# Kernel tuning notes

Hardware: AMD Instinct MI355X
Metric: run time of the kernel (lower is better)

## Reference

```python
import jax, jax.numpy as jnp
import numpy as np

K = 3  # kernel_size

def setup_inputs() -> dict:
    key = jax.random.key(0)
    k0, k1, k2 = jax.random.split(key, 3)
    B, C, H, W = 8, 128, 128, 128
    x = jax.random.normal(k0, (B, C, H, W), dtype=jnp.float32)
    # kernel_gen params: two 1x1 convs acting on a 1x1 pooled map -> plain matmuls
    w1 = jax.random.normal(k1, (C, C), dtype=jnp.float32) * 0.05          # conv1 weight [out,in]
    b1 = jnp.zeros((C,), dtype=jnp.float32)
    w2 = jax.random.normal(k2, (C * K * K, C), dtype=jnp.float32) * 0.05  # conv2 weight [out,in]
    b2 = jnp.zeros((C * K * K,), dtype=jnp.float32)
    return {"x": x, "w1": w1, "b1": b1, "w2": w2, "b2": b2}

def reference(x, w1, b1, w2, b2):
    B, C, H, W = x.shape
    k = K
    pad = k // 2
    # AdaptiveAvgPool2d(1) -> global mean; 1x1 convs -> matmuls on [B, C]
    pooled = x.mean(axis=(2, 3))                        # [B, C]
    h = jax.nn.relu(pooled @ w1.T + b1)                 # [B, C]
    kern = (h @ w2.T + b2).reshape(B, C, k * k)         # [B, C, k*k], channel-major = reshape(B*C,1,k,k)
    # Dynamic per-sample depthwise conv (cross-correlation, zero pad), via patches
    patches = jax.lax.conv_general_dilated_patches(
        x, (k, k), (1, 1), ((pad, pad), (pad, pad)),
        dimension_numbers=("NCHW", "OIHW", "NCHW"))     # [B, C*k*k, H, W], channel-major over (C, k, k)
    patches = patches.reshape(B, C, k * k, H, W)
    out = jnp.einsum("bcphw,bcp->bchw", patches, kern)  # [B, C, H, W]
    return out
```

## Files before the change

kernel.cpp:

```cpp
#include <hip/hip_runtime.h>

#define BB 8
#define CC 128
#define HH 128
#define WW 128
#define PLANE (HH * WW)
#define KK 9

__global__ __launch_bounds__(512) void pool_kernel(const float* __restrict__ x,
                                                   float* __restrict__ pooled) {
    int bc = blockIdx.x;
    const float4* p4 = (const float4*)(x + (size_t)bc * PLANE);
    int t = threadIdx.x;
    float s = 0.f;
#pragma unroll
    for (int i = 0; i < 8; ++i) {
        float4 v = p4[t + i * 512];
        s += v.x + v.y + v.z + v.w;
    }
#pragma unroll
    for (int off = 32; off > 0; off >>= 1) s += __shfl_down(s, off, 64);
    __shared__ float wsum[8];
    int wave = t >> 6, lane = t & 63;
    if (lane == 0) wsum[wave] = s;
    __syncthreads();
    if (t == 0) {
        float tot = 0.f;
#pragma unroll
        for (int i = 0; i < 8; ++i) tot += wsum[i];
        pooled[bc] = tot * (1.0f / PLANE);
    }
}

__global__ __launch_bounds__(128) void kerngen_kernel(const float* __restrict__ pooled,
                                                      const float* __restrict__ w1,
                                                      const float* __restrict__ b1,
                                                      const float* __restrict__ w2,
                                                      const float* __restrict__ b2,
                                                      float* __restrict__ kern) {
    int b = blockIdx.x / 9;
    int g = blockIdx.x % 9;
    int j = threadIdx.x;
    __shared__ float ps[CC];
    __shared__ float hs[CC];
    ps[j] = pooled[b * CC + j];
    __syncthreads();
    float acc = b1[j];
    const float* w1r = w1 + j * CC;
#pragma unroll 8
    for (int i = 0; i < CC; ++i) acc += ps[i] * w1r[i];
    hs[j] = fmaxf(acc, 0.f);
    __syncthreads();
    int o = g * CC + j;
    float acc2 = b2[o];
    const float* w2r = w2 + o * CC;
#pragma unroll 8
    for (int i = 0; i < CC; ++i) acc2 += hs[i] * w2r[i];
    kern[b * (CC * KK) + o] = acc2;
}

__global__ __launch_bounds__(256) void conv_kernel(const float* __restrict__ x,
                                                   const float* __restrict__ kern,
                                                   float* __restrict__ out) {
    int bid = blockIdx.x;
    int bc = bid >> 2, slice = bid & 3;
    const float* plane = x + (size_t)bc * PLANE;
    float* oplane = out + (size_t)bc * PLANE;
    const float* wp = kern + (size_t)bc * KK;
    float w[9];
#pragma unroll
    for (int p = 0; p < 9; ++p) w[p] = wp[p];

    int t = threadIdx.x;
    int xq = t & 31;
    int x0 = xq << 2;
    int yb = slice * 32 + (t >> 5) * 4;

    float4 A  = {0.f, 0.f, 0.f, 0.f};
    float4 Bv = {0.f, 0.f, 0.f, 0.f};

#pragma unroll
    for (int s = 0; s < 6; ++s) {
        int yr = yb - 1 + s;
        float4 cv = {0.f, 0.f, 0.f, 0.f};
        float l = 0.f, r = 0.f;
        if (yr >= 0 && yr < HH) {
            const float* row = plane + yr * WW;
            cv = *(const float4*)(row + x0);
            l = (xq > 0) ? row[x0 - 1] : 0.f;
            r = (xq < 31) ? row[x0 + 4] : 0.f;
        }
        float4 pbot, pmid, ptop;
        pbot.x = w[6]*l    + w[7]*cv.x + w[8]*cv.y;
        pbot.y = w[6]*cv.x + w[7]*cv.y + w[8]*cv.z;
        pbot.z = w[6]*cv.y + w[7]*cv.z + w[8]*cv.w;
        pbot.w = w[6]*cv.z + w[7]*cv.w + w[8]*r;
        pmid.x = w[3]*l    + w[4]*cv.x + w[5]*cv.y;
        pmid.y = w[3]*cv.x + w[4]*cv.y + w[5]*cv.z;
        pmid.z = w[3]*cv.y + w[4]*cv.z + w[5]*cv.w;
        pmid.w = w[3]*cv.z + w[4]*cv.w + w[5]*r;
        ptop.x = w[0]*l    + w[1]*cv.x + w[2]*cv.y;
        ptop.y = w[0]*cv.x + w[1]*cv.y + w[2]*cv.z;
        ptop.z = w[0]*cv.y + w[1]*cv.z + w[2]*cv.w;
        ptop.w = w[0]*cv.z + w[1]*cv.w + w[2]*r;

        A.x += pbot.x; A.y += pbot.y; A.z += pbot.z; A.w += pbot.w;
        int yo = yr - 1;
        if (yo >= yb && yo < yb + 4) {
            *(float4*)(oplane + yo * WW + x0) = A;
        }
        Bv.x += pmid.x; Bv.y += pmid.y; Bv.z += pmid.z; Bv.w += pmid.w;
        A = Bv;
        Bv = ptop;
    }
}

extern "C" void kernel_launch(void* const* d_in, const int* in_sizes, int n_in,
                              void* d_out, int out_size, void* d_ws, size_t ws_size,
                              hipStream_t stream) {
    const float* x  = (const float*)d_in[0];
    const float* w1 = (const float*)d_in[1];
    const float* b1 = (const float*)d_in[2];
    const float* w2 = (const float*)d_in[3];
    const float* b2 = (const float*)d_in[4];
    float* out = (float*)d_out;

    float* ws = (float*)d_ws;
    float* pooled = ws;
    float* kern   = ws + 1024;

    pool_kernel<<<BB * CC, 512, 0, stream>>>(x, pooled);
    kerngen_kernel<<<BB * 9, 128, 0, stream>>>(pooled, w1, b1, w2, b2, kern);
    conv_kernel<<<BB * CC * 4, 256, 0, stream>>>(x, kern, out);
}
```

Before: 138.0 us.

## Fuse pooling with kernel generation via last-block atomic counter; enlarge conv row tiles

Pooling and the kernel-generation MLP now run in one kernel. Each block publishes its plane sum, and the last block per batch, found with an atomic counter, computes the two matmuls for that batch. This removes one launch and the serial 72-block kerngen stage, at the cost of a memset launch and a single block doing each batch's 1152-output matmul. The conv kernel now has each thread produce 8 output rows instead of 4, halving the grid and cutting redundant halo-row loads.

Result: slower. 197.1 us (+42.8%).

```diff
diff --git a/kernel.cpp b/kernel.cpp
--- a/kernel.cpp
+++ b/kernel.cpp
@@ -7,64 +7,88 @@
 #define PLANE (HH * WW)
 #define KK 9
 
-__global__ __launch_bounds__(512) void pool_kernel(const float* __restrict__ x,
-                                                   float* __restrict__ pooled) {
+__global__ __launch_bounds__(512) void pool_kg_kernel(
+        const float* __restrict__ x,
+        const float* __restrict__ w1,
+        const float* __restrict__ b1,
+        const float* __restrict__ w2,
+        const float* __restrict__ b2,
+        float* __restrict__ psum,
+        int* __restrict__ counter,
+        float* __restrict__ kern) {
     int bc = blockIdx.x;
-    const float4* p4 = (const float4*)(x + (size_t)bc * PLANE);
+    int b = bc >> 7;
     int t = threadIdx.x;
+    __shared__ float wsum[8];
+    __shared__ int lastFlag;
+    __shared__ float ps[CC];
+    __shared__ float hs[CC];
+
+    const float4* g4 = (const float4*)(x + (size_t)bc * PLANE);
     float s = 0.f;
 #pragma unroll
     for (int i = 0; i < 8; ++i) {
-        float4 v = p4[t + i * 512];
+        float4 v = g4[t + i * 512];
         s += v.x + v.y + v.z + v.w;
     }
 #pragma unroll
     for (int off = 32; off > 0; off >>= 1) s += __shfl_down(s, off, 64);
-    __shared__ float wsum[8];
     int wave = t >> 6, lane = t & 63;
     if (lane == 0) wsum[wave] = s;
+    if (t == 0) lastFlag = 0;
     __syncthreads();
     if (t == 0) {
         float tot = 0.f;
 #pragma unroll
         for (int i = 0; i < 8; ++i) tot += wsum[i];
-        pooled[bc] = tot * (1.0f / PLANE);
+        __hip_atomic_store(&psum[bc], tot, __ATOMIC_RELEASE, __HIP_MEMORY_SCOPE_AGENT);
+        int old = __hip_atomic_fetch_add(&counter[b], 1, __ATOMIC_ACQ_REL,
+                                         __HIP_MEMORY_SCOPE_AGENT);
+        if (old == CC - 1) lastFlag = 1;
     }
-}
+    __syncthreads();
+    if (!lastFlag) return;
 
-__global__ __launch_bounds__(128) void kerngen_kernel(const float* __restrict__ pooled,
-                                                      const float* __restrict__ w1,
-                                                      const float* __restrict__ b1,
-                                                      const float* __restrict__ w2,
-                                                      const float* __restrict__ b2,
-                                                      float* __restrict__ kern) {
-    int b = blockIdx.x / 9;
-    int g = blockIdx.x % 9;
-    int j = threadIdx.x;
-    __shared__ float ps[CC];
-    __shared__ float hs[CC];
-    ps[j] = pooled[b * CC + j];
+    if (t < CC) {
+        float v = __hip_atomic_load(&psum[b * CC + t], __ATOMIC_ACQUIRE,
+                                    __HIP_MEMORY_SCOPE_AGENT);
+        ps[t] = v * (1.0f / PLANE);
+    }
     __syncthreads();
-    float acc = b1[j];
-    const float* w1r = w1 + j * CC;
-#pragma unroll 8
-    for (int i = 0; i < CC; ++i) acc += ps[i] * w1r[i];
-    hs[j] = fmaxf(acc, 0.f);
+
+    {
+        int j = t >> 2, k = t & 3;
+        const float* pr = ps + k * 32;
+        const float* wr = w1 + j * CC + k * 32;
+        float a = 0.f;
+#pragma unroll
+        for (int i = 0; i < 32; ++i) a += pr[i] * wr[i];
+        a += __shfl_down(a, 1, 64);
+        a += __shfl_down(a, 2, 64);
+        if (k == 0) hs[j] = fmaxf(a + b1[j], 0.f);
+    }
     __syncthreads();
-    int o = g * CC + j;
-    float acc2 = b2[o];
-    const float* w2r = w2 + o * CC;
-#pragma unroll 8
-    for (int i = 0; i < CC; ++i) acc2 += hs[i] * w2r[i];
-    kern[b * (CC * KK) + o] = acc2;
+
+    const float4* hs4 = (const float4*)hs;
+    for (int o = t; o < CC * KK; o += 512) {
+        const float4* wr4 = (const float4*)(w2 + (size_t)o * CC);
+        float a = 0.f;
+#pragma unroll
+        for (int i = 0; i < 32; ++i) {
+            float4 wv = wr4[i];
+            float4 hv = hs4[i];
+            a += wv.x * hv.x + wv.y * hv.y + wv.z * hv.z + wv.w * hv.w;
+        }
+        kern[b * (CC * KK) + o] = a + b2[o];
+    }
 }
 
 __global__ __launch_bounds__(256) void conv_kernel(const float* __restrict__ x,
                                                    const float* __restrict__ kern,
                                                    float* __restrict__ out) {
     int bid = blockIdx.x;
-    int bc = bid >> 2, slice = bid & 3;
-    const float* plane = x + (size_t)bc * PLANE;
+    int bc = bid >> 1, half = bid & 1;
+    const float* gplane = x + (size_t)bc * PLANE;
     float* oplane = out + (size_t)bc * PLANE;
     const float* wp = kern + (size_t)bc * KK;
     float w[9];
@@ -74,18 +98,18 @@
     int t = threadIdx.x;
     int xq = t & 31;
     int x0 = xq << 2;
-    int yb = slice * 32 + (t >> 5) * 4;
+    int yb = half * 64 + (t >> 5) * 8;
 
     float4 A  = {0.f, 0.f, 0.f, 0.f};
     float4 Bv = {0.f, 0.f, 0.f, 0.f};
 
 #pragma unroll
-    for (int s = 0; s < 6; ++s) {
-        int yr = yb - 1 + s;
+    for (int si = 0; si < 10; ++si) {
+        int yr = yb - 1 + si;
         float4 cv = {0.f, 0.f, 0.f, 0.f};
         float l = 0.f, r = 0.f;
         if (yr >= 0 && yr < HH) {
-            const float* row = plane + yr * WW;
+            const float* row = gplane + yr * WW;
             cv = *(const float4*)(row + x0);
             l = (xq > 0) ? row[x0 - 1] : 0.f;
             r = (xq < 31) ? row[x0 + 4] : 0.f;
@@ -105,9 +129,8 @@
         ptop.w = w[0]*cv.z + w[1]*cv.w + w[2]*r;
 
         A.x += pbot.x; A.y += pbot.y; A.z += pbot.z; A.w += pbot.w;
-        int yo = yr - 1;
-        if (yo >= yb && yo < yb + 4) {
-            *(float4*)(oplane + yo * WW + x0) = A;
+        if (si >= 2) {
+            *(float4*)(oplane + (yr - 1) * WW + x0) = A;
         }
         Bv.x += pmid.x; Bv.y += pmid.y; Bv.z += pmid.z; Bv.w += pmid.w;
         A = Bv;
@@ -125,11 +148,12 @@
     const float* b2 = (const float*)d_in[4];
     float* out = (float*)d_out;
 
-    float* ws = (float*)d_ws;
-    float* pooled = ws;
-    float* kern   = ws + 1024;
+    int*   counter = (int*)d_ws;
+    float* psum    = (float*)d_ws + 16;
+    float* kern    = psum + BB * CC;
 
-    pool_kernel<<<BB * CC, 512, 0, stream>>>(x, pooled);
-    kerngen_kernel<<<BB * 9, 128, 0, stream>>>(pooled, w1, b1, w2, b2, kern);
-    conv_kernel<<<BB * CC * 4, 256, 0, stream>>>(x, kern, out);
+    hipMemsetAsync(counter, 0, BB * sizeof(int), stream);
+    pool_kg_kernel<<<BB * CC, 512, 0, stream>>>(x, w1, b1, w2, b2,
+                                                psum, counter, kern);
+    conv_kernel<<<BB * CC * 2, 256, 0, stream>>>(x, kern, out);
 }
```
